# Performance work log

Hardware: AMD Instinct MI355X
Metric: run time of the kernel (lower is better)

## Reference

```python
import jax, jax.numpy as jnp
import numpy as np
from jax import lax

B, N, D, K = 4, 2048, 1024, 16
TAU = 16.0
LN_EPS = 1e-5


def setup_inputs() -> dict:
    key = jax.random.key(0)
    ks = jax.random.split(key, 8)
    x = jax.random.normal(ks[0], (B, N, D), dtype=jnp.float32)
    Wi = jax.random.normal(ks[1], (D, D), dtype=jnp.float32) * 0.02  # i_proj.weight [out,in]
    We = jax.random.normal(ks[2], (K, D), dtype=jnp.float32) * 0.02  # e_proj.weight
    Wf = jax.random.normal(ks[3], (D, D), dtype=jnp.float32) * 0.02  # f_proj.weight
    Ws = jax.random.normal(ks[4], (K, D), dtype=jnp.float32) * 0.02  # s_proj.weight
    gamma = jnp.ones((D,), dtype=jnp.float32)   # LayerNorm weight
    beta = jnp.zeros((D,), dtype=jnp.float32)   # LayerNorm bias
    Wo = jax.random.normal(ks[5], (D, D), dtype=jnp.float32) * 0.02  # o_proj.weight
    return {"x": x, "Wi": Wi, "We": We, "Wf": Wf, "Ws": Ws,
            "gamma": gamma, "beta": beta, "Wo": Wo}


def _forward(x, Wi, We, Wf, Ws, gamma, beta, Wo):
    # Projections (torch Linear: y = x @ W.T)
    i = jnp.einsum('bnd,ed->bne', x, Wi)          # [B,N,D]
    e = jnp.einsum('bnd,kd->bnk', x, We)          # [B,N,K]  (t_type=0: identity transform)
    s = jnp.einsum('bnd,kd->bnk', x, Ws)          # [B,N,K]
    # f_type=2, use_tau: f = exp(logsigmoid(f_proj(x)) / tau), broadcast over k
    f = jnp.exp(jax.nn.log_sigmoid(jnp.einsum('bnd,ed->bne', x, Wf)) / TAU)  # [B,N,D]

    def step(m, inp):
        i_t, e_t, f_t, s_t = inp                  # [B,D],[B,K],[B,D],[B,K]
        m = f_t[:, None, :] * m + e_t[:, :, None] * i_t[:, None, :]  # [B,K,D]
        y_t = jnp.einsum('bk,bkd->bd', s_t, m)
        return m, y_t

    xs = (jnp.swapaxes(i, 0, 1), jnp.swapaxes(e, 0, 1),
          jnp.swapaxes(f, 0, 1), jnp.swapaxes(s, 0, 1))
    m0 = jnp.zeros((B, K, D), dtype=x.dtype)
    _, ys = lax.scan(step, m0, xs)                # [N,B,D]
    y = jnp.swapaxes(ys, 0, 1)                    # [B,N,D]

    # LayerNorm then output projection
    mu = jnp.mean(y, axis=-1, keepdims=True)
    var = jnp.mean((y - mu) ** 2, axis=-1, keepdims=True)
    yn = (y - mu) * lax.rsqrt(var + LN_EPS) * gamma + beta
    return jnp.einsum('bnd,ed->bne', yn, Wo)


def reference(x, Wi, We, Wf, Ws, gamma, beta, Wo):
    return _forward(x, Wi, We, Wf, Ws, gamma, beta, Wo)
```

## Files before the change

### kernel.cpp

```cpp
#include <hip/hip_runtime.h>
#include <hip/hip_bf16.h>
#include <stdint.h>

#define B_ 4
#define N_ 2048
#define D_ 1024
#define K_ 16
#define MROWS (B_*N_)
#define NC_ 64
#define CLEN_ (N_/NC_)

typedef unsigned short u16;
typedef __attribute__((ext_vector_type(8))) short bf16x8;
typedef __attribute__((ext_vector_type(8))) short short8;
typedef __attribute__((ext_vector_type(4))) float f32x4;

__device__ __forceinline__ u16 f2bf(float f) {
  uint32_t u = __float_as_uint(f);
  u = u + 0x7fffu + ((u >> 16) & 1u);
  return (u16)(u >> 16);
}
__device__ __forceinline__ float bf2f(u16 h) {
  uint32_t u = ((uint32_t)h) << 16;
  return __uint_as_float(u);
}
__device__ __forceinline__ float fgate(float z) {
  float ls = (z >= 0.0f) ? -__logf(1.0f + __expf(-z)) : (z - __logf(1.0f + __expf(z)));
  return __expf(ls * 0.0625f);
}

__global__ __launch_bounds__(256) void cast_kernel(const float* __restrict__ in,
                                                   u16* __restrict__ out, int n) {
  int i = (blockIdx.x * 256 + threadIdx.x) * 4;
  if (i >= n) return;
  float4 v = *(const float4*)(in + i);
  ushort4 o;
  o.x = f2bf(v.x); o.y = f2bf(v.y); o.z = f2bf(v.z); o.w = f2bf(v.w);
  *(ushort4*)(out + i) = o;
}

#define GL_LDS(gp, lp) \
  __builtin_amdgcn_global_load_lds( \
      (const __attribute__((address_space(1))) void*)(gp), \
      (__attribute__((address_space(3))) void*)(lp), 16, 0, 0)

#define WAITVM(n)  asm volatile("s_waitcnt vmcnt(" #n ")" ::: "memory")
#define SCHEDB()   __builtin_amdgcn_sched_barrier(0)

__global__ __launch_bounds__(512, 1) void ring_fused(const u16* __restrict__ A,
                                                     const u16* __restrict__ W0,
                                                     const u16* __restrict__ W1,
                                                     u16* __restrict__ C0,
                                                     u16* __restrict__ C1) {
  __shared__ __align__(16) u16 lds[3 * 24576];

  const int tid = threadIdx.x;
  const int w = tid >> 6, l = tid & 63;
  const int wr = w >> 1, wc = w & 1;

  const int orig = blockIdx.x;
  const int wg = (orig & 7) * 64 + (orig >> 3);
  const int bm = wg / 16;
  const int bn = wg % 16;

  const u16* W;
  u16* C;
  int ncol0;
  if (bn >= 8) { W = W1; C = C1; ncol0 = (bn - 8) * 128; }
  else         { W = W0; C = C0; ncol0 = bn * 128; }

  const int sw = ((l & 7) ^ ((l >> 3) & 7)) * 8;
  const u16* aSrc = A + (size_t)(bm * 256 + w * 8 + (l >> 3)) * 1024 + sw;
  const u16* bSrc = W + (size_t)(ncol0 + w * 8 + (l >> 3)) * 1024 + sw;

#define STAGE_T(t, slot) do { \
    const int _sb = (slot) * 49152 + w * 1024; \
    _Pragma("unroll") \
    for (int j = 0; j < 4; ++j) \
      GL_LDS(aSrc + (size_t)j * 65536 + (t) * 64, (char*)lds + _sb + j * 8192); \
    _Pragma("unroll") \
    for (int j = 0; j < 2; ++j) \
      GL_LDS(bSrc + (size_t)j * 65536 + (t) * 64, (char*)lds + _sb + 32768 + j * 8192); \
  } while (0)

  const int sxe = (l & 7) << 3;
  const int klo = (l >> 4) * 8;
  const int aR0 = (wr * 64 + (l & 15)) * 64;
  const int bR0 = (wc * 64 + (l & 15)) * 64 + 16384;

  f32x4 acc[4][4] = {};

#define COMPUTE(slot) do { \
    const u16* S = lds + (slot) * 24576; \
    bf16x8 b0[4], a0[4], b1[4], a1[4]; \
    _Pragma("unroll") \
    for (int n = 0; n < 4; ++n) b0[n] = *(const bf16x8*)&S[bR0 + n * 1024 + (klo ^ sxe)]; \
    _Pragma("unroll") \
    for (int m = 0; m < 4; ++m) a0[m] = *(const bf16x8*)&S[aR0 + m * 1024 + (klo ^ sxe)]; \
    _Pragma("unroll") \
    for (int n = 0; n < 4; ++n) b1[n] = *(const bf16x8*)&S[bR0 + n * 1024 + ((klo + 32) ^ sxe)]; \
    _Pragma("unroll") \
    for (int m = 0; m < 4; ++m) a1[m] = *(const bf16x8*)&S[aR0 + m * 1024 + ((klo + 32) ^ sxe)]; \
    asm volatile("s_waitcnt lgkmcnt(8)" ::: "memory"); \
    SCHEDB(); \
    __builtin_amdgcn_s_setprio(1); \
    _Pragma("unroll") \
    for (int m = 0; m < 4; ++m) \
      _Pragma("unroll") \
      for (int n = 0; n < 4; ++n) \
        acc[m][n] = __builtin_amdgcn_mfma_f32_16x16x32_bf16(a0[m], b0[n], acc[m][n], 0, 0, 0); \
    __builtin_amdgcn_s_setprio(0); \
    asm volatile("s_waitcnt lgkmcnt(0)" ::: "memory"); \
    SCHEDB(); \
    __builtin_amdgcn_s_setprio(1); \
    _Pragma("unroll") \
    for (int m = 0; m < 4; ++m) \
      _Pragma("unroll") \
      for (int n = 0; n < 4; ++n) \
        acc[m][n] = __builtin_amdgcn_mfma_f32_16x16x32_bf16(a1[m], b1[n], acc[m][n], 0, 0, 0); \
    __builtin_amdgcn_s_setprio(0); \
  } while (0)

  STAGE_T(0, 0);
  STAGE_T(1, 1);
  WAITVM(6);
  __builtin_amdgcn_s_barrier();
  SCHEDB();

#pragma unroll
  for (int t = 0; t < 16; ++t) {
    if (t + 2 < 16) STAGE_T(t + 2, (t + 2) % 3);
    COMPUTE(t % 3);
    if (t < 15) {
      if (t == 14) WAITVM(0);
      else         WAITVM(6);
      __builtin_amdgcn_s_barrier();
      SCHEDB();
    }
  }

  const int orow0 = bm * 256 + wr * 64 + (l >> 4) * 4;
  const int ocol0 = ncol0 + wc * 64 + (l & 15);
#pragma unroll
  for (int m = 0; m < 4; ++m)
#pragma unroll
    for (int n = 0; n < 4; ++n)
#pragma unroll
      for (int r = 0; r < 4; ++r)
        C[(size_t)(orow0 + m * 16 + r) * 1024 + ocol0 + n * 16] = f2bf(acc[m][n][r]);
#undef STAGE_T
#undef COMPUTE
}

__global__ __launch_bounds__(256) void gemm_bt(const u16* __restrict__ A,
                                               const u16* __restrict__ W,
                                               float* __restrict__ C,
                                               int M, int N, int Kk, int epi) {
  __shared__ u16 As[128 * 32];
  __shared__ u16 Bs[128 * 32];
  const int tid = threadIdx.x;
  const int w = tid >> 6, l = tid & 63;
  const int nbn = N >> 7;
  const int bm = blockIdx.x / nbn, bn = blockIdx.x % nbn;
  const int wm = (w >> 1) * 64, wn = (w & 1) * 64;
  const int lr = l & 15, lk = (l >> 4) * 8;

  f32x4 acc[4][4] = {};

  for (int kt = 0; kt < Kk; kt += 32) {
#pragma unroll
    for (int j = 0; j < 2; ++j) {
      int ofs = w * 1024 + j * 4096;
      int gofs = ofs + l * 16;
      int row = gofs >> 6;
      int ke = (gofs & 63) >> 1;
      const u16* ga = A + (size_t)(bm * 128 + row) * Kk + kt + ke;
      const u16* gb = W + (size_t)(bn * 128 + row) * Kk + kt + ke;
      GL_LDS(ga, (char*)As + ofs);
      GL_LDS(gb, (char*)Bs + ofs);
    }
    __syncthreads();
    bf16x8 af[4], bfr[4];
#pragma unroll
    for (int i2 = 0; i2 < 4; ++i2) {
      af[i2]  = *(const bf16x8*)&As[(wm + i2 * 16 + lr) * 32 + lk];
      bfr[i2] = *(const bf16x8*)&Bs[(wn + i2 * 16 + lr) * 32 + lk];
    }
#pragma unroll
    for (int i2 = 0; i2 < 4; ++i2)
#pragma unroll
      for (int j2 = 0; j2 < 4; ++j2)
        acc[i2][j2] = __builtin_amdgcn_mfma_f32_16x16x32_bf16(af[i2], bfr[j2], acc[i2][j2], 0, 0, 0);
    __syncthreads();
  }

  const int orow0 = bm * 128 + wm + (l >> 4) * 4;
  const int ocol0 = bn * 128 + wn + (l & 15);
#pragma unroll
  for (int i2 = 0; i2 < 4; ++i2)
#pragma unroll
    for (int j2 = 0; j2 < 4; ++j2)
#pragma unroll
      for (int r = 0; r < 4; ++r)
        C[(size_t)(orow0 + i2 * 16 + r) * N + ocol0 + j2 * 16] = acc[i2][j2][r];
}

__global__ __launch_bounds__(256) void es_mfma(const u16* __restrict__ xb,
                                               const float* __restrict__ We,
                                               const float* __restrict__ Ws,
                                               float* __restrict__ e,
                                               float* __restrict__ s) {
  __shared__ __align__(16) u16 Bsm[32 * 1024];
  __shared__ __align__(16) u16 Asl[2][64 * 128];

  const int tid = threadIdx.x;
  const int w = tid >> 6, l = tid & 63;
  const int bm = blockIdx.x;

#pragma unroll
  for (int q = 0; q < 16; ++q) {
    int g = q * 256 + tid;
    int n = g >> 7;
    int c = g & 127;
    const float* src = (n < 16 ? We + (size_t)n * 1024 : Ws + (size_t)(n - 16) * 1024) + c * 8;
    float4 v0 = *(const float4*)(src);
    float4 v1 = *(const float4*)(src + 4);
    short8 o;
    o[0] = (short)f2bf(v0.x); o[1] = (short)f2bf(v0.y);
    o[2] = (short)f2bf(v0.z); o[3] = (short)f2bf(v0.w);
    o[4] = (short)f2bf(v1.x); o[5] = (short)f2bf(v1.y);
    o[6] = (short)f2bf(v1.z); o[7] = (short)f2bf(v1.w);
    *(short8*)&Bsm[(size_t)n * 1024 + (size_t)(c ^ (n & 15)) * 8] = o;
  }

  const int arow_par = w * 4 + (l >> 4);
  const int csrc = (l & 15) ^ arow_par;

#define ESTAGE(t, buf) do { \
    _Pragma("unroll") \
    for (int j = 0; j < 4; ++j) { \
      const u16* gp = xb + (size_t)(bm * 64 + j * 16 + arow_par) * 1024 + (t) * 128 + csrc * 8; \
      GL_LDS(gp, (char*)&Asl[(buf)][0] + j * 4096 + w * 1024); \
    } \
  } while (0)

  f32x4 acc[2] = {};

  ESTAGE(0, 0);
  __syncthreads();

#pragma unroll
  for (int t = 0; t < 8; ++t) {
    if (t) { WAITVM(0); __builtin_amdgcn_s_barrier(); }
    if (t + 1 < 8) ESTAGE(t + 1, (t + 1) & 1);
    const int buf = t & 1;
#pragma unroll
    for (int ks = 0; ks < 4; ++ks) {
      bf16x8 af = *(const bf16x8*)&Asl[buf][(size_t)(w * 16 + (l & 15)) * 128 +
                                           (size_t)(((ks * 4 + (l >> 4)) ^ (l & 15))) * 8];
      bf16x8 b0 = *(const bf16x8*)&Bsm[(size_t)(0 + (l & 15)) * 1024 +
                                       (size_t)(((t * 16 + ks * 4 + (l >> 4)) ^ (l & 15))) * 8];
      bf16x8 b1 = *(const bf16x8*)&Bsm[(size_t)(16 + (l & 15)) * 1024 +
                                       (size_t)(((t * 16 + ks * 4 + (l >> 4)) ^ (l & 15))) * 8];
      acc[0] = __builtin_amdgcn_mfma_f32_16x16x32_bf16(af, b0, acc[0], 0, 0, 0);
      acc[1] = __builtin_amdgcn_mfma_f32_16x16x32_bf16(af, b1, acc[1], 0, 0, 0);
    }
  }

  const int orow = bm * 64 + w * 16 + (l >> 4) * 4;
  const int ocol = l & 15;
#pragma unroll
  for (int r = 0; r < 4; ++r) {
    e[(size_t)(orow + r) * K_ + ocol] = acc[0][r];
    s[(size_t)(orow + r) * K_ + ocol] = acc[1][r];
  }
#undef ESTAGE
}

__global__ __launch_bounds__(256, 4) void scan_pass1(const u16* __restrict__ ibb,
                                                     const u16* __restrict__ zbb,
                                                     const float* __restrict__ ebuf,
                                                     float* __restrict__ Asc,
                                                     float* __restrict__ Psc) {
  __shared__ float els[CLEN_ * K_];
  int bid = blockIdx.x;
  int dq = bid & 3, c = (bid >> 2) % NC_, b = bid / (NC_ * 4);
  int d = dq * 256 + threadIdx.x;
  int t0 = c * CLEN_;

  if (threadIdx.x < CLEN_ * K_ / 4) {
    *(float4*)&els[threadIdx.x * 4] =
        *(const float4*)(ebuf + ((size_t)b * N_ + t0) * K_ + threadIdx.x * 4);
  }
  __syncthreads();

  float m[K_];
#pragma unroll
  for (int k = 0; k < K_; ++k) m[k] = 0.f;
  float p = 1.0f;
  const u16* ip = ibb + ((size_t)b * N_ + t0) * D_ + d;
  const u16* zp = zbb + ((size_t)b * N_ + t0) * D_ + d;

#pragma unroll 1
  for (int tb = 0; tb < CLEN_; tb += 8) {
    float iv[8], zv[8];
#pragma unroll
    for (int j = 0; j < 8; ++j) iv[j] = bf2f(ip[(size_t)(tb + j) * D_]);
#pragma unroll
    for (int j = 0; j < 8; ++j) zv[j] = bf2f(zp[(size_t)(tb + j) * D_]);
#pragma unroll
    for (int j = 0; j < 8; ++j) {
      float ft = fgate(zv[j]);
      p *= ft;
      const float* ec = &els[(tb + j) * K_];
#pragma unroll
      for (int k = 0; k < K_; ++k) m[k] = ft * m[k] + ec[k] * iv[j];
    }
  }

  float* ap = Asc + (((size_t)b * NC_ + c) * K_) * D_ + d;
#pragma unroll
  for (int k = 0; k < K_; ++k) ap[(size_t)k * D_] = m[k];
  Psc[((size_t)b * NC_ + c) * D_ + d] = p;
}

__global__ __launch_bounds__(256, 4) void scan_pass2(const float* __restrict__ Asc,
                                                     const float* __restrict__ Psc,
                                                     float* __restrict__ Ssc) {
  int idx = blockIdx.x * 256 + threadIdx.x;
  int d = idx & (D_ - 1);
  int k = (idx >> 10) & (K_ - 1);
  int b = idx >> 14;
  float M = 0.f;
#pragma unroll 1
  for (int cb = 0; cb < NC_; cb += 8) {
    float a[8], pp[8];
#pragma unroll
    for (int j = 0; j < 8; ++j) {
      size_t base = (((size_t)b * NC_ + cb + j) * K_ + k) * D_ + d;
      a[j] = Asc[base];
      pp[j] = Psc[((size_t)b * NC_ + cb + j) * D_ + d];
    }
#pragma unroll
    for (int j = 0; j < 8; ++j) {
      size_t base = (((size_t)b * NC_ + cb + j) * K_ + k) * D_ + d;
      Ssc[base] = M;
      M = pp[j] * M + a[j];
    }
  }
}

__global__ __launch_bounds__(256, 4) void scan_pass3(const u16* __restrict__ ibb,
                                                     const u16* __restrict__ zbb,
                                                     const float* __restrict__ ebuf,
                                                     const float* __restrict__ sbuf,
                                                     const float* __restrict__ Ssc,
                                                     u16* __restrict__ ybb) {
  __shared__ float els[CLEN_ * K_];
  __shared__ float sls[CLEN_ * K_];
  int bid = blockIdx.x;
  int dq = bid & 3, c = (bid >> 2) % NC_, b = bid / (NC_ * 4);
  int d = dq * 256 + threadIdx.x;
  int t0 = c * CLEN_;

  if (threadIdx.x < CLEN_ * K_ / 4) {
    *(float4*)&els[threadIdx.x * 4] =
        *(const float4*)(ebuf + ((size_t)b * N_ + t0) * K_ + threadIdx.x * 4);
  } else if (threadIdx.x < CLEN_ * K_ / 2) {
    int q = threadIdx.x - CLEN_ * K_ / 4;
    *(float4*)&sls[q * 4] =
        *(const float4*)(sbuf + ((size_t)b * N_ + t0) * K_ + q * 4);
  }

  float m[K_];
  const float* sp0 = Ssc + (((size_t)b * NC_ + c) * K_) * D_ + d;
#pragma unroll
  for (int k = 0; k < K_; ++k) m[k] = sp0[(size_t)k * D_];
  __syncthreads();

  const u16* ip = ibb + ((size_t)b * N_ + t0) * D_ + d;
  const u16* zp = zbb + ((size_t)b * N_ + t0) * D_ + d;
  u16* yp = ybb + ((size_t)b * N_ + t0) * D_ + d;

#pragma unroll 1
  for (int tb = 0; tb < CLEN_; tb += 8) {
    float iv[8], zv[8];
#pragma unroll
    for (int j = 0; j < 8; ++j) iv[j] = bf2f(ip[(size_t)(tb + j) * D_]);
#pragma unroll
    for (int j = 0; j < 8; ++j) zv[j] = bf2f(zp[(size_t)(tb + j) * D_]);
#pragma unroll
    for (int j = 0; j < 8; ++j) {
      float ft = fgate(zv[j]);
      const float* ec = &els[(tb + j) * K_];
      const float* sc = &sls[(tb + j) * K_];
      float y = 0.f;
#pragma unroll
      for (int k = 0; k < K_; ++k) {
        m[k] = ft * m[k] + ec[k] * iv[j];
        y += sc[k] * m[k];
      }
      yp[(size_t)(tb + j) * D_] = f2bf(y);
    }
  }
}

__global__ __launch_bounds__(256) void ln_kernel(const u16* __restrict__ y,
                                                 const float* __restrict__ gamma,
                                                 const float* __restrict__ beta,
                                                 u16* __restrict__ yn) {
  int row = blockIdx.x * 4 + (threadIdx.x >> 6);
  int l = threadIdx.x & 63;
  const u16* yr = y + (size_t)row * D_;
  float v[16];
  float sum = 0.f;
#pragma unroll
  for (int j = 0; j < 2; ++j) {
    short8 raw = *(const short8*)(yr + l * 16 + j * 8);
#pragma unroll
    for (int q = 0; q < 8; ++q) {
      float f = bf2f((u16)raw[q]);
      v[j * 8 + q] = f;
      sum += f;
    }
  }
  for (int off = 32; off > 0; off >>= 1) sum += __shfl_xor(sum, off);
  float mu = sum * (1.0f / D_);
  float vs = 0.f;
#pragma unroll
  for (int q = 0; q < 16; ++q) { float dx = v[q] - mu; vs += dx * dx; }
  for (int off = 32; off > 0; off >>= 1) vs += __shfl_xor(vs, off);
  float rstd = rsqrtf(vs * (1.0f / D_) + 1e-5f);
  int col0 = l * 16;
#pragma unroll
  for (int j = 0; j < 4; ++j) {
    float4 g = *(const float4*)(gamma + col0 + j * 4);
    float4 bt = *(const float4*)(beta + col0 + j * 4);
    ushort4 o;
    o.x = f2bf((v[j * 4 + 0] - mu) * rstd * g.x + bt.x);
    o.y = f2bf((v[j * 4 + 1] - mu) * rstd * g.y + bt.y);
    o.z = f2bf((v[j * 4 + 2] - mu) * rstd * g.z + bt.z);
    o.w = f2bf((v[j * 4 + 3] - mu) * rstd * g.w + bt.w);
    *(ushort4*)(yn + (size_t)row * D_ + col0 + j * 4) = o;
  }
}

extern "C" void kernel_launch(void* const* d_in, const int* in_sizes, int n_in,
                              void* d_out, int out_size, void* d_ws, size_t ws_size,
                              hipStream_t stream) {
  const float* x     = (const float*)d_in[0];
  const float* Wi    = (const float*)d_in[1];
  const float* We    = (const float*)d_in[2];
  const float* Wf    = (const float*)d_in[3];
  const float* Ws    = (const float*)d_in[4];
  const float* gamma = (const float*)d_in[5];
  const float* beta  = (const float*)d_in[6];
  const float* Wo    = (const float*)d_in[7];
  float* out = (float*)d_out;

  char* p = (char*)d_ws;
  u16* xb  = (u16*)p;  p += (size_t)MROWS * D_ * 2;
  u16* wib = (u16*)p;  p += (size_t)D_ * D_ * 2;
  u16* wfb = (u16*)p;  p += (size_t)D_ * D_ * 2;
  u16* wob = (u16*)p;  p += (size_t)D_ * D_ * 2;
  u16* ibb = (u16*)p;  p += (size_t)MROWS * D_ * 2;
  u16* zbb = (u16*)p;  p += (size_t)MROWS * D_ * 2;
  u16* ybb = (u16*)p;  p += (size_t)MROWS * D_ * 2;
  float* ebuf = (float*)p; p += (size_t)MROWS * K_ * 4;
  float* sbuf = (float*)p; p += (size_t)MROWS * K_ * 4;
  float* Asc  = (float*)p; p += (size_t)B_ * NC_ * K_ * D_ * 4;
  float* Ssc  = (float*)p; p += (size_t)B_ * NC_ * K_ * D_ * 4;
  float* Psc  = (float*)p; p += (size_t)B_ * NC_ * D_ * 4;

  cast_kernel<<<MROWS * D_ / 1024, 256, 0, stream>>>(x, xb, MROWS * D_);
  cast_kernel<<<D_ * D_ / 1024, 256, 0, stream>>>(Wi, wib, D_ * D_);
  cast_kernel<<<D_ * D_ / 1024, 256, 0, stream>>>(Wf, wfb, D_ * D_);
  cast_kernel<<<D_ * D_ / 1024, 256, 0, stream>>>(Wo, wob, D_ * D_);

  ring_fused<<<512, 512, 0, stream>>>(xb, wib, wfb, ibb, zbb);

  es_mfma<<<MROWS / 64, 256, 0, stream>>>(xb, We, Ws, ebuf, sbuf);

  scan_pass1<<<B_ * NC_ * 4, 256, 0, stream>>>(ibb, zbb, ebuf, Asc, Psc);
  scan_pass2<<<B_ * K_ * D_ / 256, 256, 0, stream>>>(Asc, Psc, Ssc);
  scan_pass3<<<B_ * NC_ * 4, 256, 0, stream>>>(ibb, zbb, ebuf, sbuf, Ssc, ybb);

  u16* ynb = xb;
  ln_kernel<<<MROWS / 4, 256, 0, stream>>>(ybb, gamma, beta, ynb);

  gemm_bt<<<512, 256, 0, stream>>>(ynb, wob, out, MROWS, D_, D_, 0);
}
```

Baseline: 179.5 us.

## Fold LayerNorm into output GEMM epilogue, halve scan chunks, in-place scan carry

```diff
diff --git a/kernel.cpp b/kernel.cpp
--- a/kernel.cpp
+++ b/kernel.cpp
@@ -7,7 +7,7 @@
 #define D_ 1024
 #define K_ 16
 #define MROWS (B_*N_)
-#define NC_ 64
+#define NC_ 32
 #define CLEN_ (N_/NC_)
 
 typedef unsigned short u16;
@@ -39,6 +39,38 @@
   *(ushort4*)(out + i) = o;
 }
 
+__global__ __launch_bounds__(256) void prep_kernel(const float* __restrict__ Wo,
+                                                   const float* __restrict__ gamma,
+                                                   const float* __restrict__ beta,
+                                                   u16* __restrict__ Wg,
+                                                   float* __restrict__ u,
+                                                   float* __restrict__ v) {
+  __shared__ float red[8];
+  int c = blockIdx.x;
+  int tid = threadIdx.x;
+  int k0 = tid * 4;
+  float4 wv = *(const float4*)(Wo + (size_t)c * D_ + k0);
+  float4 g4 = *(const float4*)(gamma + k0);
+  float4 b4 = *(const float4*)(beta + k0);
+  ushort4 o;
+  o.x = f2bf(wv.x * g4.x); o.y = f2bf(wv.y * g4.y);
+  o.z = f2bf(wv.z * g4.z); o.w = f2bf(wv.w * g4.w);
+  *(ushort4*)(Wg + (size_t)c * D_ + k0) = o;
+  float us = wv.x * g4.x + wv.y * g4.y + wv.z * g4.z + wv.w * g4.w;
+  float vs = wv.x * b4.x + wv.y * b4.y + wv.z * b4.z + wv.w * b4.w;
+  for (int off = 32; off > 0; off >>= 1) {
+    us += __shfl_xor(us, off);
+    vs += __shfl_xor(vs, off);
+  }
+  int w = tid >> 6, l = tid & 63;
+  if (l == 0) { red[w] = us; red[4 + w] = vs; }
+  __syncthreads();
+  if (tid == 0) {
+    u[c] = red[0] + red[1] + red[2] + red[3];
+    v[c] = red[4] + red[5] + red[6] + red[7];
+  }
+}
+
 #define GL_LDS(gp, lp) \
   __builtin_amdgcn_global_load_lds( \
       (const __attribute__((address_space(1))) void*)(gp), \
@@ -152,30 +184,34 @@
 #undef COMPUTE
 }
 
-__global__ __launch_bounds__(256) void gemm_bt(const u16* __restrict__ A,
-                                               const u16* __restrict__ W,
-                                               float* __restrict__ C,
-                                               int M, int N, int Kk, int epi) {
+__global__ __launch_bounds__(256) void gemm_bt_ln(const u16* __restrict__ A,
+                                                  const u16* __restrict__ W,
+                                                  float* __restrict__ C,
+                                                  const float* __restrict__ rstd,
+                                                  const float* __restrict__ mrs,
+                                                  const float* __restrict__ u,
+                                                  const float* __restrict__ v) {
   __shared__ u16 As[128 * 32];
   __shared__ u16 Bs[128 * 32];
   const int tid = threadIdx.x;
   const int w = tid >> 6, l = tid & 63;
-  const int nbn = N >> 7;
-  const int bm = blockIdx.x / nbn, bn = blockIdx.x % nbn;
+  const int orig = blockIdx.x;
+  const int swz = (orig & 7) * 64 + (orig >> 3);
+  const int bm = swz >> 3, bn = swz & 7;
   const int wm = (w >> 1) * 64, wn = (w & 1) * 64;
   const int lr = l & 15, lk = (l >> 4) * 8;
 
   f32x4 acc[4][4] = {};
 
-  for (int kt = 0; kt < Kk; kt += 32) {
+  for (int kt = 0; kt < 1024; kt += 32) {
 #pragma unroll
     for (int j = 0; j < 2; ++j) {
       int ofs = w * 1024 + j * 4096;
       int gofs = ofs + l * 16;
       int row = gofs >> 6;
       int ke = (gofs & 63) >> 1;
-      const u16* ga = A + (size_t)(bm * 128 + row) * Kk + kt + ke;
-      const u16* gb = W + (size_t)(bn * 128 + row) * Kk + kt + ke;
+      const u16* ga = A + (size_t)(bm * 128 + row) * 1024 + kt + ke;
+      const u16* gb = W + (size_t)(bn * 128 + row) * 1024 + kt + ke;
       GL_LDS(ga, (char*)As + ofs);
       GL_LDS(gb, (char*)Bs + ofs);
     }
@@ -197,12 +233,18 @@
   const int orow0 = bm * 128 + wm + (l >> 4) * 4;
   const int ocol0 = bn * 128 + wn + (l & 15);
 #pragma unroll
-  for (int i2 = 0; i2 < 4; ++i2)
-#pragma unroll
-    for (int j2 = 0; j2 < 4; ++j2)
-#pragma unroll
-      for (int r = 0; r < 4; ++r)
-        C[(size_t)(orow0 + i2 * 16 + r) * N + ocol0 + j2 * 16] = acc[i2][j2][r];
+  for (int i2 = 0; i2 < 4; ++i2) {
+#pragma unroll
+    for (int j2 = 0; j2 < 4; ++j2) {
+      int col = ocol0 + j2 * 16;
+      float uc = u[col], vc = v[col];
+#pragma unroll
+      for (int r = 0; r < 4; ++r) {
+        int row = orow0 + i2 * 16 + r;
+        C[(size_t)row * 1024 + col] = rstd[row] * acc[i2][j2][r] + mrs[row] * uc + vc;
+      }
+    }
+  }
 }
 
 __global__ __launch_bounds__(256) void es_mfma(const u16* __restrict__ xb,
@@ -288,10 +330,8 @@
   int d = dq * 256 + threadIdx.x;
   int t0 = c * CLEN_;
 
-  if (threadIdx.x < CLEN_ * K_ / 4) {
-    *(float4*)&els[threadIdx.x * 4] =
-        *(const float4*)(ebuf + ((size_t)b * N_ + t0) * K_ + threadIdx.x * 4);
-  }
+  *(float4*)&els[threadIdx.x * 4] =
+      *(const float4*)(ebuf + ((size_t)b * N_ + t0) * K_ + threadIdx.x * 4);
   __syncthreads();
 
   float m[K_];
@@ -324,9 +364,8 @@
   Psc[((size_t)b * NC_ + c) * D_ + d] = p;
 }
 
-__global__ __launch_bounds__(256, 4) void scan_pass2(const float* __restrict__ Asc,
-                                                     const float* __restrict__ Psc,
-                                                     float* __restrict__ Ssc) {
+__global__ __launch_bounds__(256, 4) void scan_pass2(float* __restrict__ Asc,
+                                                     const float* __restrict__ Psc) {
   int idx = blockIdx.x * 256 + threadIdx.x;
   int d = idx & (D_ - 1);
   int k = (idx >> 10) & (K_ - 1);
@@ -344,7 +383,7 @@
 #pragma unroll
     for (int j = 0; j < 8; ++j) {
       size_t base = (((size_t)b * NC_ + cb + j) * K_ + k) * D_ + d;
-      Ssc[base] = M;
+      Asc[base] = M;
       M = pp[j] * M + a[j];
     }
   }
@@ -363,14 +402,10 @@
   int d = dq * 256 + threadIdx.x;
   int t0 = c * CLEN_;
 
-  if (threadIdx.x < CLEN_ * K_ / 4) {
-    *(float4*)&els[threadIdx.x * 4] =
-        *(const float4*)(ebuf + ((size_t)b * N_ + t0) * K_ + threadIdx.x * 4);
-  } else if (threadIdx.x < CLEN_ * K_ / 2) {
-    int q = threadIdx.x - CLEN_ * K_ / 4;
-    *(float4*)&sls[q * 4] =
-        *(const float4*)(sbuf + ((size_t)b * N_ + t0) * K_ + q * 4);
-  }
+  *(float4*)&els[threadIdx.x * 4] =
+      *(const float4*)(ebuf + ((size_t)b * N_ + t0) * K_ + threadIdx.x * 4);
+  *(float4*)&sls[threadIdx.x * 4] =
+      *(const float4*)(sbuf + ((size_t)b * N_ + t0) * K_ + threadIdx.x * 4);
 
   float m[K_];
   const float* sp0 = Ssc + (((size_t)b * NC_ + c) * K_) * D_ + d;
@@ -405,43 +440,33 @@
   }
 }
 
-__global__ __launch_bounds__(256) void ln_kernel(const u16* __restrict__ y,
-                                                 const float* __restrict__ gamma,
-                                                 const float* __restrict__ beta,
-                                                 u16* __restrict__ yn) {
+__global__ __launch_bounds__(256) void rowstat(const u16* __restrict__ y,
+                                               float* __restrict__ rstd,
+                                               float* __restrict__ mrs) {
   int row = blockIdx.x * 4 + (threadIdx.x >> 6);
   int l = threadIdx.x & 63;
   const u16* yr = y + (size_t)row * D_;
-  float v[16];
-  float sum = 0.f;
+  float sum = 0.f, sq = 0.f;
 #pragma unroll
   for (int j = 0; j < 2; ++j) {
     short8 raw = *(const short8*)(yr + l * 16 + j * 8);
 #pragma unroll
     for (int q = 0; q < 8; ++q) {
       float f = bf2f((u16)raw[q]);
-      v[j * 8 + q] = f;
       sum += f;
-    }
-  }
-  for (int off = 32; off > 0; off >>= 1) sum += __shfl_xor(sum, off);
-  float mu = sum * (1.0f / D_);
-  float vs = 0.f;
-#pragma unroll
-  for (int q = 0; q < 16; ++q) { float dx = v[q] - mu; vs += dx * dx; }
-  for (int off = 32; off > 0; off >>= 1) vs += __shfl_xor(vs, off);
-  float rstd = rsqrtf(vs * (1.0f / D_) + 1e-5f);
-  int col0 = l * 16;
-#pragma unroll
-  for (int j = 0; j < 4; ++j) {
-    float4 g = *(const float4*)(gamma + col0 + j * 4);
-    float4 bt = *(const float4*)(beta + col0 + j * 4);
-    ushort4 o;
-    o.x = f2bf((v[j * 4 + 0] - mu) * rstd * g.x + bt.x);
-    o.y = f2bf((v[j * 4 + 1] - mu) * rstd * g.y + bt.y);
-    o.z = f2bf((v[j * 4 + 2] - mu) * rstd * g.z + bt.z);
-    o.w = f2bf((v[j * 4 + 3] - mu) * rstd * g.w + bt.w);
-    *(ushort4*)(yn + (size_t)row * D_ + col0 + j * 4) = o;
+      sq += f * f;
+    }
+  }
+  for (int off = 32; off > 0; off >>= 1) {
+    sum += __shfl_xor(sum, off);
+    sq  += __shfl_xor(sq, off);
+  }
+  if (l == 0) {
+    float mu = sum * (1.0f / D_);
+    float var = sq * (1.0f / D_) - mu * mu;
+    float rs = rsqrtf(var + 1e-5f);
+    rstd[row] = rs;
+    mrs[row] = -mu * rs;
   }
 }
 
@@ -459,34 +484,36 @@
   float* out = (float*)d_out;
 
   char* p = (char*)d_ws;
-  u16* xb  = (u16*)p;  p += (size_t)MROWS * D_ * 2;
-  u16* wib = (u16*)p;  p += (size_t)D_ * D_ * 2;
-  u16* wfb = (u16*)p;  p += (size_t)D_ * D_ * 2;
-  u16* wob = (u16*)p;  p += (size_t)D_ * D_ * 2;
-  u16* ibb = (u16*)p;  p += (size_t)MROWS * D_ * 2;
-  u16* zbb = (u16*)p;  p += (size_t)MROWS * D_ * 2;
-  u16* ybb = (u16*)p;  p += (size_t)MROWS * D_ * 2;
+  u16* xb   = (u16*)p;  p += (size_t)MROWS * D_ * 2;
+  u16* wib  = (u16*)p;  p += (size_t)D_ * D_ * 2;
+  u16* wfb  = (u16*)p;  p += (size_t)D_ * D_ * 2;
+  u16* wgb  = (u16*)p;  p += (size_t)D_ * D_ * 2;
+  u16* ibb  = (u16*)p;  p += (size_t)MROWS * D_ * 2;
+  u16* zbb  = (u16*)p;  p += (size_t)MROWS * D_ * 2;
+  u16* ybb  = (u16*)p;  p += (size_t)MROWS * D_ * 2;
   float* ebuf = (float*)p; p += (size_t)MROWS * K_ * 4;
   float* sbuf = (float*)p; p += (size_t)MROWS * K_ * 4;
   float* Asc  = (float*)p; p += (size_t)B_ * NC_ * K_ * D_ * 4;
-  float* Ssc  = (float*)p; p += (size_t)B_ * NC_ * K_ * D_ * 4;
   float* Psc  = (float*)p; p += (size_t)B_ * NC_ * D_ * 4;
+  float* rstd = (float*)p; p += (size_t)MROWS * 4;
+  float* mrs  = (float*)p; p += (size_t)MROWS * 4;
+  float* ub   = (float*)p; p += (size_t)D_ * 4;
+  float* vb   = (float*)p; p += (size_t)D_ * 4;
 
   cast_kernel<<<MROWS * D_ / 1024, 256, 0, stream>>>(x, xb, MROWS * D_);
   cast_kernel<<<D_ * D_ / 1024, 256, 0, stream>>>(Wi, wib, D_ * D_);
   cast_kernel<<<D_ * D_ / 1024, 256, 0, stream>>>(Wf, wfb, D_ * D_);
-  cast_kernel<<<D_ * D_ / 1024, 256, 0, stream>>>(Wo, wob, D_ * D_);
+  prep_kernel<<<D_, 256, 0, stream>>>(Wo, gamma, beta, wgb, ub, vb);
 
   ring_fused<<<512, 512, 0, stream>>>(xb, wib, wfb, ibb, zbb);
 
   es_mfma<<<MROWS / 64, 256, 0, stream>>>(xb, We, Ws, ebuf, sbuf);
 
   scan_pass1<<<B_ * NC_ * 4, 256, 0, stream>>>(ibb, zbb, ebuf, Asc, Psc);
-  scan_pass2<<<B_ * K_ * D_ / 256, 256, 0, stream>>>(Asc, Psc, Ssc);
-  scan_pass3<<<B_ * NC_ * 4, 256, 0, stream>>>(ibb, zbb, ebuf, sbuf, Ssc, ybb);
-
-  u16* ynb = xb;
-  ln_kernel<<<MROWS / 4, 256, 0, stream>>>(ybb, gamma, beta, ynb);
-
-  gemm_bt<<<512, 256, 0, stream>>>(ynb, wob, out, MROWS, D_, D_, 0);
-}
+  scan_pass2<<<B_ * K_ * D_ / 256, 256, 0, stream>>>(Asc, Psc);
+  scan_pass3<<<B_ * NC_ * 4, 256, 0, stream>>>(ibb, zbb, ebuf, sbuf, Asc, ybb);
+
+  rowstat<<<MROWS / 4, 256, 0, stream>>>(ybb, rstd, mrs);
+
+  gemm_bt_ln<<<512, 256, 0, stream>>>(ybb, wgb, out, rstd, mrs, ub, vb);
+}
```

New measurement: 182.1 us. No clear change (+1.5%).
